# Optimization experiments

Measured on AMD Instinct MI355X. Metric: run time of the kernel, lower is better.

The kernel has to match this reference:

```python
import jax, jax.numpy as jnp
import numpy as np

V_PER_MESH = 6596
HIDDEN = 128
# per-body-part clamp limits from the original module (parts 1..14)
LIMITS = jnp.array([0.04, 0.06, 0.04, 0.04, 0.02, 0.02, 0.04, 0.04,
                    0.03, 0.03, 0.02, 0.02, 0.01, 0.01], dtype=jnp.float32)


def setup_inputs() -> dict:
    key = jax.random.key(0)
    ks = jax.random.split(key, 16)
    B, V, H = 32, V_PER_MESH, HIDDEN
    N = B * V
    E = 3 * N
    inp = {}
    inp["verts"] = jax.random.normal(ks[0], (N, 3), jnp.float32)
    inp["normals"] = jax.random.normal(ks[1], (N, 3), jnp.float32)
    inp["anchor_v"] = jax.random.uniform(ks[2], (V, 3), jnp.float32)
    inp["edges"] = jax.random.randint(ks[3], (E, 2), 0, N)
    inp["part_id"] = jax.random.randint(ks[4], (V,), 0, 14)
    dims = [3, H + 3, H + 3]  # first gconv sees only vert normals (vert_feat_dim=0)
    i = 5
    for l, d in enumerate(dims):
        s = 1.0 / np.sqrt(d)
        inp[f"w0_{l}"] = jax.random.normal(ks[i], (d, H), jnp.float32) * s; i += 1
        inp[f"b0_{l}"] = jnp.zeros((H,), jnp.float32)
        inp[f"w1_{l}"] = jax.random.normal(ks[i], (d, H), jnp.float32) * s; i += 1
        inp[f"b1_{l}"] = jnp.zeros((H,), jnp.float32)
    inp["w_off"] = jax.random.normal(ks[i], (H + 3, 3), jnp.float32) * 0.01
    inp["b_off"] = jnp.zeros((3,), jnp.float32)
    return inp


def _forward(verts, normals, anchor_v, edges, part_id, layers, w_off, b_off):
    N = verts.shape[0]
    B = N // V_PER_MESH
    e0, e1 = edges[:, 0], edges[:, 1]
    feats = normals  # vert_pos_packed (verts_normals_packed), vert_feats=None
    for (w0, b0, w1, b1) in layers:
        x0 = feats @ w0 + b0            # [N,H] self transform
        x1 = feats @ w1 + b1            # [N,H] neighbor transform
        # undirected gather-scatter over mesh edges
        nbr = jnp.zeros_like(x0).at[e0].add(x1[e1]).at[e1].add(x1[e0])
        h = jax.nn.relu(x0 + nbr)       # vert_feats_nopos
        feats = jnp.concatenate([h, normals], axis=1)  # [N,H+3]
    deform = jnp.tanh(feats @ w_off + b_off)  # [N,3]
    # per-body-part clamp, vectorized: one limit per vertex, tiled over meshes
    lim = jnp.tile(LIMITS[part_id], B)[:, None]          # [N,1]
    clamped = jnp.clip(deform, -lim, lim)
    anchor = jnp.tile(anchor_v, (B, 1))                  # [N,3]
    new_verts = verts + clamped * anchor                 # offset_verts
    return new_verts, h


def reference(verts, normals, anchor_v, edges, part_id,
              w0_0, b0_0, w1_0, b1_0,
              w0_1, b0_1, w1_1, b1_1,
              w0_2, b0_2, w1_2, b1_2,
              w_off, b_off):
    layers = [(w0_0, b0_0, w1_0, b1_0),
              (w0_1, b0_1, w1_1, b1_1),
              (w0_2, b0_2, w1_2, b1_2)]
    return _forward(verts, normals, anchor_v, edges, part_id, layers, w_off, b_off)
```

## Files before the change

kernel.cpp:

```cpp
#include <hip/hip_runtime.h>

#define N_TOT 211072
#define V_MESH 6596
#define E_TOT 633216
#define CAP 32
#define KD 264
#define KSTEPS 8

typedef __attribute__((ext_vector_type(8))) short bf16x8;
typedef __attribute__((ext_vector_type(4))) float f32x4;

__constant__ float c_LIM[14] = {0.04f,0.06f,0.04f,0.04f,0.02f,0.02f,0.04f,0.04f,
                                0.03f,0.03f,0.02f,0.02f,0.01f,0.01f};

__device__ __forceinline__ unsigned f2bf(float f) {
    unsigned x = __float_as_uint(f);
    return (x + 0x7fffu + ((x >> 16) & 1u)) >> 16;
}
__device__ __forceinline__ float bflo(unsigned u) { return __uint_as_float(u << 16); }
__device__ __forceinline__ float bfhi(unsigned u) { return __uint_as_float(u & 0xffff0000u); }
__device__ __forceinline__ unsigned cvt_pk_bf16(float lo, float hi) {
    unsigned r;
    asm("v_cvt_pk_bf16_f32 %0, %1, %2" : "=v"(r) : "v"(lo), "v"(hi));
    return r;
}

__global__ __launch_bounds__(256) void fill_adj_kernel(const int* __restrict__ edges,
                                                       int* __restrict__ cnt,
                                                       int* __restrict__ adj) {
    int e = blockIdx.x * 256 + threadIdx.x;
    if (e >= E_TOT) return;
    int2 ed = ((const int2*)edges)[e];
    int p0 = atomicAdd(&cnt[ed.x], 1);
    if (p0 < CAP) adj[(size_t)ed.x * CAP + p0] = ed.y;
    int p1 = atomicAdd(&cnt[ed.y], 1);
    if (p1 < CAP) adj[(size_t)ed.y * CAP + p1] = ed.x;
}

__global__ __launch_bounds__(256) void pad_adj_kernel(const int* __restrict__ cnt,
                                                      int* __restrict__ adj) {
    int i = blockIdx.x * 256 + threadIdx.x;
    if (i >= N_TOT) return;
    int deg = cnt[i]; if (deg > CAP) deg = CAP;
    for (int k = deg; k < CAP; ++k) adj[(size_t)i * CAP + k] = N_TOT;
}

__global__ __launch_bounds__(256) void prep_nrm4_kernel(const float* __restrict__ normals,
                                                        float4* __restrict__ nrm4) {
    int i = blockIdx.x * 256 + threadIdx.x;
    if (i > N_TOT) return;
    float4 v = {0.f, 0.f, 0.f, 0.f};
    if (i < N_TOT) {
        v.x = normals[(size_t)i * 3 + 0];
        v.y = normals[(size_t)i * 3 + 1];
        v.z = normals[(size_t)i * 3 + 2];
    }
    nrm4[i] = v;
}

__global__ __launch_bounds__(256) void nsum_kernel(const float4* __restrict__ nrm4,
                                                   const int* __restrict__ cnt,
                                                   const int* __restrict__ adj,
                                                   float4* __restrict__ SS) {
    int i = blockIdx.x * 256 + threadIdx.x;
    if (i >= N_TOT) return;
    int deg = cnt[i]; if (deg > CAP) deg = CAP;
    const int4* a4 = (const int4*)(adj + (size_t)i * CAP);
    int4 A = a4[0], B = a4[1];
    float4 n0 = nrm4[A.x], n1 = nrm4[A.y], n2 = nrm4[A.z], n3 = nrm4[A.w];
    float4 m0 = nrm4[B.x], m1 = nrm4[B.y], m2 = nrm4[B.z], m3 = nrm4[B.w];
    float sx = ((n0.x + n1.x) + (n2.x + n3.x)) + ((m0.x + m1.x) + (m2.x + m3.x));
    float sy = ((n0.y + n1.y) + (n2.y + n3.y)) + ((m0.y + m1.y) + (m2.y + m3.y));
    float sz = ((n0.z + n1.z) + (n2.z + n3.z)) + ((m0.z + m1.z) + (m2.z + m3.z));
    for (int bq = 8; bq < deg; bq += 8) {
        int4 C = a4[bq / 4], D = a4[bq / 4 + 1];
        float4 p0 = nrm4[C.x], p1 = nrm4[C.y], p2 = nrm4[C.z], p3 = nrm4[C.w];
        float4 q0 = nrm4[D.x], q1 = nrm4[D.y], q2 = nrm4[D.z], q3 = nrm4[D.w];
        sx += ((p0.x + p1.x) + (p2.x + p3.x)) + ((q0.x + q1.x) + (q2.x + q3.x));
        sy += ((p0.y + p1.y) + (p2.y + p3.y)) + ((q0.y + q1.y) + (q2.y + q3.y));
        sz += ((p0.z + p1.z) + (p2.z + p3.z)) + ((q0.z + q1.z) + (q2.z + q3.z));
    }
    float4 out; out.x = sx; out.y = sy; out.z = sz; out.w = (float)deg;
    SS[i] = out;
}

__global__ __launch_bounds__(256) void conv_w2_kernel(const float* __restrict__ w0,
                                                      const float* __restrict__ b0,
                                                      const float* __restrict__ w1,
                                                      const float* __restrict__ b1,
                                                      short* __restrict__ Wt,
                                                      float4* __restrict__ hdA,
                                                      float4* __restrict__ hdB) {
    int c = blockIdx.x;
    for (int k = threadIdx.x; k < KD; k += 256) {
        unsigned val = 0u;
        if (k < 128)      val = f2bf(w0[(size_t)k * 128 + c]);
        else if (k < 256) val = f2bf(w1[(size_t)(k - 128) * 128 + c]);
        Wt[(size_t)c * KD + k] = (short)val;
    }
    if (threadIdx.x == 0) {
        hdA[c] = make_float4(b0[c], b1[c], w0[128 * 128 + c], w0[129 * 128 + c]);
        hdB[c] = make_float4(w0[130 * 128 + c], w1[128 * 128 + c],
                             w1[129 * 128 + c], w1[130 * 128 + c]);
    }
}

__global__ __launch_bounds__(1024) void fused1_kernel(const float4* __restrict__ nrm4,
                                                      const float4* __restrict__ SS,
                                                      const float* __restrict__ w0,
                                                      const float* __restrict__ b0,
                                                      const float* __restrict__ w1,
                                                      const float* __restrict__ b1,
                                                      unsigned* __restrict__ hout) {
    __shared__ float wL[2][3][128];
    __shared__ float bL[2][128];
    int tid  = threadIdx.x;
    int w    = tid >> 6;
    int lane = tid & 63;
    int i    = blockIdx.x * 16 + w;

    if (tid < 768) {
        int mm = tid / 384, r = tid - mm * 384;
        (&wL[mm][0][0])[r] = (mm ? w1 : w0)[r];
    } else if (tid < 1024) {
        int t2 = tid - 768;
        if (t2 < 256) bL[t2 >> 7][t2 & 127] = ((t2 >> 7) ? b1 : b0)[t2 & 127];
    }
    float4 self4 = nrm4[i];
    float4 S4 = SS[i];
    float degf = S4.w;
    __syncthreads();

    int c0 = 2 * lane, c1 = 2 * lane + 1;
    float h0 = bL[0][c0] + degf * bL[1][c0]
             + self4.x * wL[0][0][c0] + self4.y * wL[0][1][c0] + self4.z * wL[0][2][c0]
             + S4.x * wL[1][0][c0] + S4.y * wL[1][1][c0] + S4.z * wL[1][2][c0];
    float h1 = bL[0][c1] + degf * bL[1][c1]
             + self4.x * wL[0][0][c1] + self4.y * wL[0][1][c1] + self4.z * wL[0][2][c1]
             + S4.x * wL[1][0][c1] + S4.y * wL[1][1][c1] + S4.z * wL[1][2][c1];
    hout[(size_t)i * 64 + lane] = cvt_pk_bf16(fmaxf(h0, 0.f), fmaxf(h1, 0.f));
}

template<int LAST>
__global__ __launch_bounds__(512, 8) void fused2_kernel(const unsigned* __restrict__ hin,
                                                        const float4* __restrict__ nrm4,
                                                        const float4* __restrict__ SS,
                                                        const int* __restrict__ cnt,
                                                        const int* __restrict__ adj,
                                                        const short* __restrict__ Wt,
                                                        const float4* __restrict__ hdA,
                                                        const float4* __restrict__ hdB,
                                                        unsigned* __restrict__ hnext,
                                                        const float* __restrict__ verts,
                                                        const float* __restrict__ anchor_v,
                                                        const int* __restrict__ part_id,
                                                        const float* __restrict__ w_off,
                                                        const float* __restrict__ b_off,
                                                        float* __restrict__ houtf,
                                                        float* __restrict__ out_verts) {
    __shared__ short tileA[16 * KD];
    __shared__ unsigned tileC[16 * 64];
    __shared__ float headL[16][8];
    __shared__ float woL[131 * 3];
    __shared__ float partL[8][16][3];

    int tid  = threadIdx.x;
    int w    = tid >> 6;
    int lane = tid & 63;
    int g    = lane >> 4;
    int ln   = lane & 15;
    int row0 = blockIdx.x * 16;
    int rA   = 2 * w, rB = 2 * w + 1;
    int iA   = row0 + rA, iB = row0 + rB;

    if (LAST) {
        for (int t = tid; t < 131 * 3; t += 512) woL[t] = w_off[t];
    }

    int node = (lane < 32) ? iA : iB;
    int jv = adj[(size_t)node * CAP + (lane & 31)];
    int degA = cnt[iA]; degA = (degA > CAP) ? CAP : degA;
    int degB = cnt[iB]; degB = (degB > CAP) ? CAP : degB;
    unsigned selfA = hin[(size_t)iA * 64 + lane];
    unsigned selfB = hin[(size_t)iB * 64 + lane];
    float4 nn = nrm4[node];
    float4 sv = SS[node];
    if ((lane & 31) == 0) {
        int r = rA + (lane >> 5);
        headL[r][0] = nn.x; headL[r][1] = nn.y; headL[r][2] = nn.z; headL[r][3] = sv.w;
        headL[r][4] = sv.x; headL[r][5] = sv.y; headL[r][6] = sv.z; headL[r][7] = 0.f;
    }

    const unsigned* hb = hin + lane;
    unsigned uA[8], uB[8];
    #pragma unroll
    for (int q = 0; q < 8; ++q) {
        int jA = __builtin_amdgcn_readlane(jv, q);
        int jB = __builtin_amdgcn_readlane(jv, 32 + q);
        uA[q] = hb[(size_t)jA * 64];
        uB[q] = hb[(size_t)jB * 64];
    }
    float sA0 = 0.f, sA1 = 0.f, sB0 = 0.f, sB1 = 0.f;
    #pragma unroll
    for (int q = 0; q < 8; ++q) {
        sA0 += bflo(uA[q]); sA1 += bfhi(uA[q]);
        sB0 += bflo(uB[q]); sB1 += bfhi(uB[q]);
    }
    degA = __builtin_amdgcn_readfirstlane(degA);
    degB = __builtin_amdgcn_readfirstlane(degB);
    int degM = (degA > degB) ? degA : degB;
    for (int bq = 8; bq < degM; bq += 8) {
        unsigned vA[8], vB[8];
        #pragma unroll
        for (int q = 0; q < 8; ++q) {
            int jA = __builtin_amdgcn_readlane(jv, bq + q);
            int jB = __builtin_amdgcn_readlane(jv, 32 + bq + q);
            vA[q] = hb[(size_t)jA * 64];
            vB[q] = hb[(size_t)jB * 64];
        }
        #pragma unroll
        for (int q = 0; q < 8; ++q) {
            sA0 += bflo(vA[q]); sA1 += bfhi(vA[q]);
            sB0 += bflo(vB[q]); sB1 += bfhi(vB[q]);
        }
    }

    unsigned* tA = (unsigned*)tileA;
    tA[rA * 132 + lane]      = selfA;
    tA[rB * 132 + lane]      = selfB;
    tA[rA * 132 + 64 + lane] = cvt_pk_bf16(sA0, sA1);
    tA[rB * 132 + 64 + lane] = cvt_pk_bf16(sB0, sB1);
    if (lane < 4) {
        tA[rA * 132 + 128 + lane] = 0u;
        tA[rB * 132 + 128 + lane] = 0u;
    }
    __syncthreads();

    int cb = w * 16, c = cb + ln;
    float4 hA = hdA[c], hB = hdB[c];
    bf16x8 bfrag[KSTEPS];
    #pragma unroll
    for (int kk = 0; kk < KSTEPS; ++kk)
        bfrag[kk] = *(const bf16x8*)(Wt + (size_t)c * KD + kk * 32 + g * 8);

    f32x4 acc;
    #pragma unroll
    for (int j = 0; j < 4; ++j) {
        int r = g * 4 + j;
        acc[j] = hA.x + headL[r][3] * hA.y
               + headL[r][0] * hA.z + headL[r][1] * hA.w + headL[r][2] * hB.x
               + headL[r][4] * hB.y + headL[r][5] * hB.z + headL[r][6] * hB.w;
    }
    #pragma unroll
    for (int kk = 0; kk < KSTEPS; ++kk) {
        bf16x8 af = *(const bf16x8*)(tileA + ln * KD + kk * 32 + g * 8);
        acc = __builtin_amdgcn_mfma_f32_16x16x32_bf16(af, bfrag[kk], acc, 0, 0, 0);
    }
    #pragma unroll
    for (int j = 0; j < 4; ++j) acc[j] = fmaxf(acc[j], 0.f);

    if (!LAST) {
        #pragma unroll
        for (int j = 0; j < 4; ++j) {
            float po = __shfl_xor(acc[j], 1);
            if (!(ln & 1)) {
                unsigned pk = cvt_pk_bf16(acc[j], po);
                int r = g * 4 + j;
                int d = (cb + ln) >> 1;
                tileC[r * 64 + (d ^ ((r & 12) << 1))] = pk;
            }
        }
        __syncthreads();
        int r2 = 2 * w + (lane >> 5);
        int d2 = (lane & 31) * 2;
        int key = (r2 & 12) << 1;
        uint2 v2 = *(const uint2*)&tileC[r2 * 64 + (d2 ^ key)];
        *(uint2*)(hnext + (size_t)(row0 + r2) * 64 + d2) = v2;
    } else {
        #pragma unroll
        for (int j = 0; j < 4; ++j) {
            int r = g * 4 + j;
            float p0 = acc[j] * woL[c * 3 + 0];
            float p1 = acc[j] * woL[c * 3 + 1];
            float p2 = acc[j] * woL[c * 3 + 2];
            #pragma unroll
            for (int d = 1; d < 16; d <<= 1) {
                p0 += __shfl_xor(p0, d);
                p1 += __shfl_xor(p1, d);
                p2 += __shfl_xor(p2, d);
            }
            if (ln == 0) {
                partL[w][r][0] = p0; partL[w][r][1] = p1; partL[w][r][2] = p2;
            }
        }
        __syncthreads();
        float* tCf = (float*)tileA;
        #pragma unroll
        for (int j = 0; j < 4; ++j) {
            int r = g * 4 + j;
            tCf[r * 132 + c] = acc[j];
        }
        __syncthreads();
        {
            int r = tid >> 5, c4 = (tid & 31) * 4;
            float4 v = *(const float4*)&tCf[r * 132 + c4];
            *(float4*)(houtf + (size_t)(row0 + r) * 128 + c4) = v;
        }
        if (tid < 48) {
            int r = tid / 3, t = tid - r * 3;
            int i = row0 + r;
            float s = 0.f;
            #pragma unroll
            for (int ww = 0; ww < 8; ++ww) s += partL[ww][r][t];
            s += headL[r][0] * woL[128 * 3 + t] + headL[r][1] * woL[129 * 3 + t]
               + headL[r][2] * woL[130 * 3 + t] + b_off[t];
            float dd = tanhf(s);
            int v = i % V_MESH;
            float lim = c_LIM[part_id[v]];
            dd = fminf(fmaxf(dd, -lim), lim);
            out_verts[(size_t)i * 3 + t] =
                verts[(size_t)i * 3 + t] + dd * anchor_v[(size_t)v * 3 + t];
        }
    }
}

extern "C" void kernel_launch(void* const* d_in, const int* in_sizes, int n_in,
                              void* d_out, int out_size, void* d_ws, size_t ws_size,
                              hipStream_t stream) {
    const float* verts    = (const float*)d_in[0];
    const float* normals  = (const float*)d_in[1];
    const float* anchor_v = (const float*)d_in[2];
    const int*   edges    = (const int*)d_in[3];
    const int*   part_id  = (const int*)d_in[4];
    const float* w0_0 = (const float*)d_in[5];
    const float* b0_0 = (const float*)d_in[6];
    const float* w1_0 = (const float*)d_in[7];
    const float* b1_0 = (const float*)d_in[8];
    const float* w0_1 = (const float*)d_in[9];
    const float* b0_1 = (const float*)d_in[10];
    const float* w1_1 = (const float*)d_in[11];
    const float* b1_1 = (const float*)d_in[12];
    const float* w0_2 = (const float*)d_in[13];
    const float* b0_2 = (const float*)d_in[14];
    const float* w1_2 = (const float*)d_in[15];
    const float* b1_2 = (const float*)d_in[16];
    const float* w_off = (const float*)d_in[17];
    const float* b_off = (const float*)d_in[18];

    float* out_verts = (float*)d_out;
    float* houtf = (float*)d_out + (size_t)3 * N_TOT;

    char* p = (char*)d_ws;
    unsigned* h1 = (unsigned*)p;   p += (size_t)(N_TOT + 1) * 64 * 4;
    unsigned* h2 = (unsigned*)p;   p += (size_t)(N_TOT + 1) * 64 * 4;
    int*    cnt  = (int*)p;        p += (size_t)N_TOT * 4;
    int*    adj  = (int*)p;        p += (size_t)N_TOT * CAP * 4;
    short*  Wt1  = (short*)p;      p += 128 * KD * 2;
    short*  Wt2  = (short*)p;      p += 128 * KD * 2;
    float4* hdA1 = (float4*)p;     p += 128 * 16;
    float4* hdB1 = (float4*)p;     p += 128 * 16;
    float4* hdA2 = (float4*)p;     p += 128 * 16;
    float4* hdB2 = (float4*)p;     p += 128 * 16;
    float4* nrm4 = (float4*)p;     p += (size_t)(N_TOT + 1) * 16;
    float4* SS   = (float4*)p;     p += (size_t)N_TOT * 16;

    hipMemsetAsync(cnt, 0, (size_t)N_TOT * 4, stream);
    hipMemsetAsync(h1 + (size_t)N_TOT * 64, 0, 256, stream);
    hipMemsetAsync(h2 + (size_t)N_TOT * 64, 0, 256, stream);
    fill_adj_kernel<<<(E_TOT + 255) / 256, 256, 0, stream>>>(edges, cnt, adj);
    pad_adj_kernel<<<(N_TOT + 255) / 256, 256, 0, stream>>>(cnt, adj);
    prep_nrm4_kernel<<<(N_TOT + 256) / 256, 256, 0, stream>>>(normals, nrm4);
    conv_w2_kernel<<<128, 256, 0, stream>>>(w0_1, b0_1, w1_1, b1_1, Wt1, hdA1, hdB1);
    conv_w2_kernel<<<128, 256, 0, stream>>>(w0_2, b0_2, w1_2, b1_2, Wt2, hdA2, hdB2);
    nsum_kernel<<<(N_TOT + 255) / 256, 256, 0, stream>>>(nrm4, cnt, adj, SS);

    fused1_kernel<<<N_TOT / 16, 1024, 0, stream>>>(nrm4, SS, w0_0, b0_0, w1_0, b1_0, h1);
    fused2_kernel<0><<<N_TOT / 16, 512, 0, stream>>>(h1, nrm4, SS, cnt, adj, Wt1, hdA1, hdB1,
                                                     h2, nullptr, nullptr, nullptr, nullptr,
                                                     nullptr, nullptr, nullptr);
    fused2_kernel<1><<<N_TOT / 16, 512, 0, stream>>>(h2, nrm4, SS, cnt, adj, Wt2, hdA2, hdB2,
                                                     nullptr, verts, anchor_v, part_id,
                                                     w_off, b_off, houtf, out_verts);
}
```

Before: 419.8 us.

## Double fused2 block rows and replace padding kernel with sentinel index -1 memset

The fused layer kernel now processes 32 rows per block with 1024 threads, with two row-halves sharing the loaded weight fragments and head data. The adjacency padding kernel is dropped: adj is memset to 0xFF so empty slots read index -1. The zero sentinel row moves to the front of h1, h2 and nrm4 through offset base pointers. This removes one kernel launch and reuses per-block setup over more rows, at the cost of a full-size memset of adj and heavier per-block shared memory and register pressure.

```diff
diff --git a/kernel.cpp b/kernel.cpp
--- a/kernel.cpp
+++ b/kernel.cpp
@@ -37,24 +37,15 @@
     if (p1 < CAP) adj[(size_t)ed.y * CAP + p1] = ed.x;
 }
 
-__global__ __launch_bounds__(256) void pad_adj_kernel(const int* __restrict__ cnt,
-                                                      int* __restrict__ adj) {
-    int i = blockIdx.x * 256 + threadIdx.x;
-    if (i >= N_TOT) return;
-    int deg = cnt[i]; if (deg > CAP) deg = CAP;
-    for (int k = deg; k < CAP; ++k) adj[(size_t)i * CAP + k] = N_TOT;
-}
-
 __global__ __launch_bounds__(256) void prep_nrm4_kernel(const float* __restrict__ normals,
                                                         float4* __restrict__ nrm4) {
     int i = blockIdx.x * 256 + threadIdx.x;
-    if (i > N_TOT) return;
-    float4 v = {0.f, 0.f, 0.f, 0.f};
-    if (i < N_TOT) {
-        v.x = normals[(size_t)i * 3 + 0];
-        v.y = normals[(size_t)i * 3 + 1];
-        v.z = normals[(size_t)i * 3 + 2];
-    }
+    if (i >= N_TOT) return;
+    float4 v;
+    v.x = normals[(size_t)i * 3 + 0];
+    v.y = normals[(size_t)i * 3 + 1];
+    v.z = normals[(size_t)i * 3 + 2];
+    v.w = 0.f;
     nrm4[i] = v;
 }
 
@@ -142,39 +133,39 @@
 }
 
 template<int LAST>
-__global__ __launch_bounds__(512, 8) void fused2_kernel(const unsigned* __restrict__ hin,
-                                                        const float4* __restrict__ nrm4,
-                                                        const float4* __restrict__ SS,
-                                                        const int* __restrict__ cnt,
-                                                        const int* __restrict__ adj,
-                                                        const short* __restrict__ Wt,
-                                                        const float4* __restrict__ hdA,
-                                                        const float4* __restrict__ hdB,
-                                                        unsigned* __restrict__ hnext,
-                                                        const float* __restrict__ verts,
-                                                        const float* __restrict__ anchor_v,
-                                                        const int* __restrict__ part_id,
-                                                        const float* __restrict__ w_off,
-                                                        const float* __restrict__ b_off,
-                                                        float* __restrict__ houtf,
-                                                        float* __restrict__ out_verts) {
-    __shared__ short tileA[16 * KD];
-    __shared__ unsigned tileC[16 * 64];
-    __shared__ float headL[16][8];
+__global__ __launch_bounds__(1024, 8) void fused2_kernel(const unsigned* __restrict__ hin,
+                                                         const float4* __restrict__ nrm4,
+                                                         const float4* __restrict__ SS,
+                                                         const int* __restrict__ cnt,
+                                                         const int* __restrict__ adj,
+                                                         const short* __restrict__ Wt,
+                                                         const float4* __restrict__ hdA,
+                                                         const float4* __restrict__ hdB,
+                                                         unsigned* __restrict__ hnext,
+                                                         const float* __restrict__ verts,
+                                                         const float* __restrict__ anchor_v,
+                                                         const int* __restrict__ part_id,
+                                                         const float* __restrict__ w_off,
+                                                         const float* __restrict__ b_off,
+                                                         float* __restrict__ houtf,
+                                                         float* __restrict__ out_verts) {
+    __shared__ short tileA[32 * KD];
+    __shared__ unsigned tileC[32 * 64];
+    __shared__ float headL[32][8];
     __shared__ float woL[131 * 3];
-    __shared__ float partL[8][16][3];
+    __shared__ float partL[8][32][3];
 
     int tid  = threadIdx.x;
     int w    = tid >> 6;
     int lane = tid & 63;
     int g    = lane >> 4;
     int ln   = lane & 15;
-    int row0 = blockIdx.x * 16;
+    int row0 = blockIdx.x * 32;
     int rA   = 2 * w, rB = 2 * w + 1;
     int iA   = row0 + rA, iB = row0 + rB;
 
     if (LAST) {
-        for (int t = tid; t < 131 * 3; t += 512) woL[t] = w_off[t];
+        for (int t = tid; t < 131 * 3; t += 1024) woL[t] = w_off[t];
     }
 
     int node = (lane < 32) ? iA : iB;
@@ -197,8 +188,8 @@
     for (int q = 0; q < 8; ++q) {
         int jA = __builtin_amdgcn_readlane(jv, q);
         int jB = __builtin_amdgcn_readlane(jv, 32 + q);
-        uA[q] = hb[(size_t)jA * 64];
-        uB[q] = hb[(size_t)jB * 64];
+        uA[q] = hb[(ptrdiff_t)jA * 64];
+        uB[q] = hb[(ptrdiff_t)jB * 64];
     }
     float sA0 = 0.f, sA1 = 0.f, sB0 = 0.f, sB1 = 0.f;
     #pragma unroll
@@ -215,8 +206,8 @@
         for (int q = 0; q < 8; ++q) {
             int jA = __builtin_amdgcn_readlane(jv, bq + q);
             int jB = __builtin_amdgcn_readlane(jv, 32 + bq + q);
-            vA[q] = hb[(size_t)jA * 64];
-            vB[q] = hb[(size_t)jB * 64];
+            vA[q] = hb[(ptrdiff_t)jA * 64];
+            vB[q] = hb[(ptrdiff_t)jB * 64];
         }
         #pragma unroll
         for (int q = 0; q < 8; ++q) {
@@ -236,7 +227,8 @@
     }
     __syncthreads();
 
-    int cb = w * 16, c = cb + ln;
+    int rh = w >> 3;
+    int cb = (w & 7) * 16, c = cb + ln;
     float4 hA = hdA[c], hB = hdB[c];
     bf16x8 bfrag[KSTEPS];
     #pragma unroll
@@ -246,14 +238,14 @@
     f32x4 acc;
     #pragma unroll
     for (int j = 0; j < 4; ++j) {
-        int r = g * 4 + j;
+        int r = rh * 16 + g * 4 + j;
         acc[j] = hA.x + headL[r][3] * hA.y
                + headL[r][0] * hA.z + headL[r][1] * hA.w + headL[r][2] * hB.x
                + headL[r][4] * hB.y + headL[r][5] * hB.z + headL[r][6] * hB.w;
     }
     #pragma unroll
     for (int kk = 0; kk < KSTEPS; ++kk) {
-        bf16x8 af = *(const bf16x8*)(tileA + ln * KD + kk * 32 + g * 8);
+        bf16x8 af = *(const bf16x8*)(tileA + (rh * 16 + ln) * KD + kk * 32 + g * 8);
         acc = __builtin_amdgcn_mfma_f32_16x16x32_bf16(af, bfrag[kk], acc, 0, 0, 0);
     }
     #pragma unroll
@@ -265,7 +257,7 @@
             float po = __shfl_xor(acc[j], 1);
             if (!(ln & 1)) {
                 unsigned pk = cvt_pk_bf16(acc[j], po);
-                int r = g * 4 + j;
+                int r = rh * 16 + g * 4 + j;
                 int d = (cb + ln) >> 1;
                 tileC[r * 64 + (d ^ ((r & 12) << 1))] = pk;
             }
@@ -279,7 +271,7 @@
     } else {
         #pragma unroll
         for (int j = 0; j < 4; ++j) {
-            int r = g * 4 + j;
+            int r = rh * 16 + g * 4 + j;
             float p0 = acc[j] * woL[c * 3 + 0];
             float p1 = acc[j] * woL[c * 3 + 1];
             float p2 = acc[j] * woL[c * 3 + 2];
@@ -290,14 +282,14 @@
                 p2 += __shfl_xor(p2, d);
             }
             if (ln == 0) {
-                partL[w][r][0] = p0; partL[w][r][1] = p1; partL[w][r][2] = p2;
+                partL[w & 7][r][0] = p0; partL[w & 7][r][1] = p1; partL[w & 7][r][2] = p2;
             }
         }
         __syncthreads();
         float* tCf = (float*)tileA;
         #pragma unroll
         for (int j = 0; j < 4; ++j) {
-            int r = g * 4 + j;
+            int r = rh * 16 + g * 4 + j;
             tCf[r * 132 + c] = acc[j];
         }
         __syncthreads();
@@ -306,7 +298,7 @@
             float4 v = *(const float4*)&tCf[r * 132 + c4];
             *(float4*)(houtf + (size_t)(row0 + r) * 128 + c4) = v;
         }
-        if (tid < 48) {
+        if (tid < 96) {
             int r = tid / 3, t = tid - r * 3;
             int i = row0 + r;
             float s = 0.f;
@@ -351,8 +343,8 @@
     float* houtf = (float*)d_out + (size_t)3 * N_TOT;
 
     char* p = (char*)d_ws;
-    unsigned* h1 = (unsigned*)p;   p += (size_t)(N_TOT + 1) * 64 * 4;
-    unsigned* h2 = (unsigned*)p;   p += (size_t)(N_TOT + 1) * 64 * 4;
+    unsigned* h1b = (unsigned*)p;  p += (size_t)(N_TOT + 1) * 64 * 4;
+    unsigned* h2b = (unsigned*)p;  p += (size_t)(N_TOT + 1) * 64 * 4;
     int*    cnt  = (int*)p;        p += (size_t)N_TOT * 4;
     int*    adj  = (int*)p;        p += (size_t)N_TOT * CAP * 4;
     short*  Wt1  = (short*)p;      p += 128 * KD * 2;
@@ -361,24 +353,29 @@
     float4* hdB1 = (float4*)p;     p += 128 * 16;
     float4* hdA2 = (float4*)p;     p += 128 * 16;
     float4* hdB2 = (float4*)p;     p += 128 * 16;
-    float4* nrm4 = (float4*)p;     p += (size_t)(N_TOT + 1) * 16;
+    float4* nrm4b = (float4*)p;    p += (size_t)(N_TOT + 1) * 16;
     float4* SS   = (float4*)p;     p += (size_t)N_TOT * 16;
 
+    unsigned* h1 = h1b + 64;
+    unsigned* h2 = h2b + 64;
+    float4* nrm4 = nrm4b + 1;
+
     hipMemsetAsync(cnt, 0, (size_t)N_TOT * 4, stream);
-    hipMemsetAsync(h1 + (size_t)N_TOT * 64, 0, 256, stream);
-    hipMemsetAsync(h2 + (size_t)N_TOT * 64, 0, 256, stream);
+    hipMemsetAsync(h1b, 0, 256, stream);
+    hipMemsetAsync(h2b, 0, 256, stream);
+    hipMemsetAsync(nrm4b, 0, 16, stream);
+    hipMemsetAsync(adj, 0xFF, (size_t)N_TOT * CAP * 4, stream);
     fill_adj_kernel<<<(E_TOT + 255) / 256, 256, 0, stream>>>(edges, cnt, adj);
-    pad_adj_kernel<<<(N_TOT + 255) / 256, 256, 0, stream>>>(cnt, adj);
-    prep_nrm4_kernel<<<(N_TOT + 256) / 256, 256, 0, stream>>>(normals, nrm4);
+    prep_nrm4_kernel<<<(N_TOT + 255) / 256, 256, 0, stream>>>(normals, nrm4);
     conv_w2_kernel<<<128, 256, 0, stream>>>(w0_1, b0_1, w1_1, b1_1, Wt1, hdA1, hdB1);
     conv_w2_kernel<<<128, 256, 0, stream>>>(w0_2, b0_2, w1_2, b1_2, Wt2, hdA2, hdB2);
     nsum_kernel<<<(N_TOT + 255) / 256, 256, 0, stream>>>(nrm4, cnt, adj, SS);
 
     fused1_kernel<<<N_TOT / 16, 1024, 0, stream>>>(nrm4, SS, w0_0, b0_0, w1_0, b1_0, h1);
-    fused2_kernel<0><<<N_TOT / 16, 512, 0, stream>>>(h1, nrm4, SS, cnt, adj, Wt1, hdA1, hdB1,
-                                                     h2, nullptr, nullptr, nullptr, nullptr,
-                                                     nullptr, nullptr, nullptr);
-    fused2_kernel<1><<<N_TOT / 16, 512, 0, stream>>>(h2, nrm4, SS, cnt, adj, Wt2, hdA2, hdB2,
-                                                     nullptr, verts, anchor_v, part_id,
-                                                     w_off, b_off, houtf, out_verts);
-}
+    fused2_kernel<0><<<N_TOT / 32, 1024, 0, stream>>>(h1, nrm4, SS, cnt, adj, Wt1, hdA1, hdB1,
+                                                      h2, nullptr, nullptr, nullptr, nullptr,
+                                                      nullptr, nullptr, nullptr);
+    fused2_kernel<1><<<N_TOT / 32, 1024, 0, stream>>>(h2, nrm4, SS, cnt, adj, Wt2, hdA2, hdB2,
+                                                      nullptr, verts, anchor_v, part_id,
+                                                      w_off, b_off, houtf, out_verts);
+}
```

Result: no change. 423.0 us (+0.8%).
